# Optimization experiments

Hardware: AMD Instinct MI355X
Metric: run time of the kernel (lower is better)

## Reference

```python
import jax, jax.numpy as jnp
import numpy as np

N = 100000     # total nodes in batch
E = 1600000    # total edges in batch
G = 1024       # number of graphs in batch
IN, H1, H2, FC, OUT = 128, 128, 128, 128, 1


def setup_inputs() -> dict:
    key = jax.random.key(0)
    ks = jax.random.split(key, 8)
    node_feats = jax.random.normal(ks[0], (N, IN), jnp.float32)
    adj = jax.random.randint(ks[1], (2, E), 0, N)
    graph_idx = jnp.sort(jax.random.randint(ks[2], (N,), 0, G))
    init = lambda k, sh, fan: jax.random.normal(k, sh, jnp.float32) / np.float32(np.sqrt(fan))
    W1 = init(ks[3], (IN, H1), IN); b1 = jnp.zeros((H1,), jnp.float32)
    W2 = init(ks[4], (H1, H2), H1); b2 = jnp.zeros((H2,), jnp.float32)
    Wfc = init(ks[5], (H2, FC), H2); bfc = jnp.zeros((FC,), jnp.float32)
    Wout = init(ks[6], (FC, OUT), FC); bout = jnp.zeros((OUT,), jnp.float32)
    return dict(node_feats=node_feats, adj=adj, graph_idx=graph_idx, is_training=0,
                W1=W1, b1=b1, W2=W2, b2=b2, Wfc=Wfc, bfc=bfc, Wout=Wout, bout=bout)


def _gcn_layer(x, src, dst, W, b):
    # h = relu( D^{-1/2} A D^{-1/2} (x W + b) ), A given as an edge list (src -> dst)
    h = x @ W + b                                   # [N, H]
    ones = jnp.ones((src.shape[0],), h.dtype)
    deg = jax.ops.segment_sum(ones, dst, num_segments=N)      # node degrees
    norm = jnp.where(deg > 0, jax.lax.rsqrt(jnp.maximum(deg, 1.0)), 0.0)
    msg = h[src] * norm[src][:, None]               # gather over edges [E, H]
    agg = jax.ops.segment_sum(msg, dst, num_segments=N) * norm[:, None]
    return jax.nn.relu(agg)


def reference(node_feats, adj, graph_idx, is_training, W1, b1, W2, b2, Wfc, bfc, Wout, bout):
    src, dst = adj[0], adj[1]
    h = _gcn_layer(node_feats, src, dst, W1, b1)
    h = _gcn_layer(h, src, dst, W2, b2)
    # mean pooling per graph (segment mean)
    counts = jax.ops.segment_sum(jnp.ones((N,), h.dtype), graph_idx, num_segments=G)
    graph_feat = jax.ops.segment_sum(h, graph_idx, num_segments=G) / jnp.maximum(counts, 1.0)[:, None]
    # MLP head (predicator_dropout = 0.0, is_training=False -> no dropout)
    graph_feat = jax.nn.relu(graph_feat @ Wfc + bfc)
    return graph_feat @ Wout + bout                 # [G, n_out]
```

## Files before the change

### kernel.cpp

```cpp
#include <hip/hip_runtime.h>


typedef unsigned short ushort_t;
typedef unsigned int   uint_t;
typedef unsigned char  uchar_t;
typedef __attribute__((ext_vector_type(8))) short bf16x8;
typedef __attribute__((ext_vector_type(4))) float f32x4;
typedef __attribute__((ext_vector_type(2))) float f32x2;

#define EPB     4096
#define CAP2    32
#define BKT_CAP 8192

__device__ __forceinline__ float bf2f(uint_t u) { return __uint_as_float(u << 16); }
__device__ __forceinline__ ushort_t f2bf(float f) {
  uint_t x = __float_as_uint(f);
  x = x + 0x7fffu + ((x >> 16) & 1u);
  return (ushort_t)(x >> 16);
}

__device__ __forceinline__ bf16x8 pack8(float4 u, float4 v) {
  union { uint4 q; bf16x8 b; } cv;
  cv.q.x = (uint_t)f2bf(u.x) | ((uint_t)f2bf(u.y) << 16);
  cv.q.y = (uint_t)f2bf(u.z) | ((uint_t)f2bf(u.w) << 16);
  cv.q.z = (uint_t)f2bf(v.x) | ((uint_t)f2bf(v.y) << 16);
  cv.q.w = (uint_t)f2bf(v.z) | ((uint_t)f2bf(v.w) << 16);
  return cv.b;
}

__global__ __launch_bounds__(256, 4) void k_front(const float* __restrict__ X, const float* __restrict__ W1,
                                                  const float* __restrict__ b1, uchar_t* __restrict__ Yf8,
                                                  uchar_t* __restrict__ YfC,
                                                  const float* __restrict__ W2, ushort_t* __restrict__ Wf2,
                                                  const int* __restrict__ src, const int* __restrict__ dst,
                                                  uint_t* __restrict__ binbuf, int* __restrict__ cntmatT,
                                                  int E, int N, int nblk, int nbkt, int GB1) {
  __shared__ ushort_t Ws[16384];
  __shared__ int cur[512];
  int t = threadIdx.x;
  int bid = blockIdx.x;

  if (bid < nblk) {
    for (int r = t; r < nbkt; r += 256) cur[r] = 0;
    __syncthreads();
    int base = bid * EPB;
#pragma unroll
    for (int j = 0; j < EPB / 256; j++) {
      int e = base + j * 256 + t;
      if (e < E) {
        int s = src[e], d = dst[e];
        int b = d >> 8;
        int p = atomicAdd(&cur[b], 1);
        if (p < CAP2)
          binbuf[((size_t)b * nblk + bid) * CAP2 + p] = (uint_t)s | ((uint_t)(d & 255) << 17);
      }
    }
    __syncthreads();
    for (int r = t; r < nbkt; r += 256) {
      int c = cur[r];
      cntmatT[(size_t)r * nblk + bid] = (c < CAP2) ? c : CAP2;
    }
    return;
  }
  if (bid < nblk + 64) {
    if (bid == nblk && t < 8)  ((uint4*)Yf8)[(size_t)N * 8 + t] = make_uint4(0u, 0u, 0u, 0u);
    if (bid == nblk && t >= 8 && t < 16)
      ((uint4*)YfC)[(size_t)N * 8 + (t - 8)] = make_uint4(0u, 0u, 0u, 0u);
    int idx = (bid - nblk) * 256 + t;
    int n = idx & 127, k = idx >> 7;
    Wf2[((size_t)(k >> 3) * 128 + n) * 8 + (k & 7)] = f2bf(W2[(size_t)k * 128 + n]);
    return;
  }

  {
    const float4* W4 = (const float4*)W1;
#pragma unroll
    for (int i = 0; i < 16; i++) {
      int idx = i * 256 + t;
      int k = idx >> 5;
      int n0 = (idx & 31) * 4;
      float4 v = W4[idx];
      int qb = k >> 3, j = k & 7;
      Ws[((size_t)qb * 128 + n0 + 0) * 8 + j] = f2bf(v.x);
      Ws[((size_t)qb * 128 + n0 + 1) * 8 + j] = f2bf(v.y);
      Ws[((size_t)qb * 128 + n0 + 2) * 8 + j] = f2bf(v.z);
      Ws[((size_t)qb * 128 + n0 + 3) * 8 + j] = f2bf(v.w);
    }
  }
  int r0 = (bid - nblk - 64) * 128;
  int wave = t >> 6, lane = t & 63;
  int ln = lane & 15, quad = lane >> 4;
  int row0 = r0 + wave * 32 + ln;
  int row1 = row0 + 16;
  int cr0 = min(row0, N - 1);
  int cr1 = min(row1, N - 1);

  bf16x8 a0[4], a1[4];
  {
    const float4* Xp = (const float4*)X;
#pragma unroll
    for (int kc = 0; kc < 4; kc++) {
      int q = kc * 4 + quad;
      float4 u0 = Xp[(size_t)cr0 * 32 + q * 2];
      float4 v0 = Xp[(size_t)cr0 * 32 + q * 2 + 1];
      float4 u1 = Xp[(size_t)cr1 * 32 + q * 2];
      float4 v1 = Xp[(size_t)cr1 * 32 + q * 2 + 1];
      a0[kc] = pack8(u0, v0);
      a1[kc] = pack8(u1, v1);
    }
  }
  __syncthreads();

  const bf16x8* Wb = (const bf16x8*)Ws;
  f32x4 acc[2][8];
#pragma unroll
  for (int mt = 0; mt < 2; mt++)
#pragma unroll
    for (int ct = 0; ct < 8; ct++) acc[mt][ct] = (f32x4){0.f, 0.f, 0.f, 0.f};

#pragma unroll
  for (int kc = 0; kc < 4; kc++) {
    int q = kc * 4 + quad;
#pragma unroll
    for (int ct = 0; ct < 8; ct++) {
      bf16x8 b = Wb[q * 128 + ct * 16 + ln];
      acc[0][ct] = __builtin_amdgcn_mfma_f32_16x16x32_bf16(b, a0[kc], acc[0][ct], 0, 0, 0);
      acc[1][ct] = __builtin_amdgcn_mfma_f32_16x16x32_bf16(b, a1[kc], acc[1][ct], 0, 0, 0);
    }
  }

  int chbase = quad * 4;
  float4 bs[8];
#pragma unroll
  for (int ct = 0; ct < 8; ct++) bs[ct] = *(const float4*)(b1 + ct * 16 + chbase);
  uint_t* Y32 = (uint_t*)Yf8;
  if (row0 < N) {
#pragma unroll
    for (int ct = 0; ct < 8; ct++) {
      f32x4 v = acc[0][ct];
      float x0 = (v[0] + bs[ct].x) * 16.f, x1 = (v[1] + bs[ct].y) * 16.f;
      float x2 = (v[2] + bs[ct].z) * 16.f, x3 = (v[3] + bs[ct].w) * 16.f;
      int w = __builtin_amdgcn_cvt_pk_fp8_f32(x0, x1, 0, false);
      w = __builtin_amdgcn_cvt_pk_fp8_f32(x2, x3, w, true);
      Y32[(size_t)row0 * 32 + ct * 4 + quad] = (uint_t)w;
    }
  }
  if (row1 < N) {
#pragma unroll
    for (int ct = 0; ct < 8; ct++) {
      f32x4 v = acc[1][ct];
      float x0 = (v[0] + bs[ct].x) * 16.f, x1 = (v[1] + bs[ct].y) * 16.f;
      float x2 = (v[2] + bs[ct].z) * 16.f, x3 = (v[3] + bs[ct].w) * 16.f;
      int w = __builtin_amdgcn_cvt_pk_fp8_f32(x0, x1, 0, false);
      w = __builtin_amdgcn_cvt_pk_fp8_f32(x2, x3, w, true);
      Y32[(size_t)row1 * 32 + ct * 4 + quad] = (uint_t)w;
    }
  }
}

__global__ __launch_bounds__(512) void k_csr(const uint_t* __restrict__ binbuf, const int* __restrict__ cntmatT,
                                             int* __restrict__ esrc, int* __restrict__ deg,
                                             int* __restrict__ offs, float* __restrict__ nrm,
                                             int N, int nblk) {
  __shared__ int cnt_s[512];
  __shared__ int hist[256];
  __shared__ int cur[256];
  __shared__ int wsum[4];
  __shared__ int lsrc[BKT_CAP];
  int b = blockIdx.x, t = threadIdx.x;
  if (b == 0 && t == 0) nrm[N] = 0.f;
  int n0 = b << 8;
  int gbase = b * BKT_CAP;
  for (int r = t; r < nblk; r += 512) cnt_s[r] = cntmatT[(size_t)b * nblk + r];
  if (t < 256) hist[t] = 0;
  __syncthreads();
  const uint4* seg4 = (const uint4*)(binbuf + (size_t)b * nblk * CAP2);
  int total4 = (nblk * CAP2) >> 2;
  for (int i4 = t; i4 < total4; i4 += 512) {
    int base = i4 << 2;
    int c = cnt_s[base >> 5];
    int s0 = base & 31;
    if (s0 < c) {
      uint4 v = seg4[i4];
      int nv = c - s0;
      atomicAdd(&hist[v.x >> 17], 1);
      if (nv > 1) atomicAdd(&hist[v.y >> 17], 1);
      if (nv > 2) atomicAdd(&hist[v.z >> 17], 1);
      if (nv > 3) atomicAdd(&hist[v.w >> 17], 1);
    }
  }
  __syncthreads();
  int lane = t & 63, wv = t >> 6;
  if (t < 256) {
    int h = hist[t];
    int incl = h;
#pragma unroll
    for (int s = 1; s < 64; s <<= 1) {
      int x = __shfl_up(incl, s, 64);
      if (lane >= s) incl += x;
    }
    if (lane == 63) wsum[wv] = incl;
    __syncthreads();
    int wbase = 0;
#pragma unroll
    for (int k = 0; k < 4; k++) wbase += (k < wv) ? wsum[k] : 0;
    int excl = wbase + incl - h;
    cur[t] = excl;
    int node = n0 + t;
    if (node < N) {
      deg[node] = h;
      offs[node] = gbase + excl;
      nrm[node] = (h > 0) ? rsqrtf((float)h) : 0.f;
    }
  } else {
    __syncthreads();
  }
  __syncthreads();
  int count = wsum[0] + wsum[1] + wsum[2] + wsum[3];
  for (int i4 = t; i4 < total4; i4 += 512) {
    int base = i4 << 2;
    int c = cnt_s[base >> 5];
    int s0 = base & 31;
    if (s0 < c) {
      uint4 v = seg4[i4];
      int nv = c - s0;
      { int p = atomicAdd(&cur[v.x >> 17], 1); lsrc[p] = (int)(v.x & 0x1ffffu); }
      if (nv > 1) { int p = atomicAdd(&cur[v.y >> 17], 1); lsrc[p] = (int)(v.y & 0x1ffffu); }
      if (nv > 2) { int p = atomicAdd(&cur[v.z >> 17], 1); lsrc[p] = (int)(v.z & 0x1ffffu); }
      if (nv > 3) { int p = atomicAdd(&cur[v.w >> 17], 1); lsrc[p] = (int)(v.w & 0x1ffffu); }
    }
  }
  __syncthreads();
  for (int i = t; i < count; i += 512) esrc[gbase + i] = lsrc[i];
}

__device__ __forceinline__ void acc16p(f32x2* a, uint4 g) {
  a[0] += __builtin_amdgcn_cvt_pk_f32_fp8((int)g.x, false);
  a[1] += __builtin_amdgcn_cvt_pk_f32_fp8((int)g.x, true);
  a[2] += __builtin_amdgcn_cvt_pk_f32_fp8((int)g.y, false);
  a[3] += __builtin_amdgcn_cvt_pk_f32_fp8((int)g.y, true);
  a[4] += __builtin_amdgcn_cvt_pk_f32_fp8((int)g.z, false);
  a[5] += __builtin_amdgcn_cvt_pk_f32_fp8((int)g.z, true);
  a[6] += __builtin_amdgcn_cvt_pk_f32_fp8((int)g.w, false);
  a[7] += __builtin_amdgcn_cvt_pk_f32_fp8((int)g.w, true);
}
__device__ __forceinline__ void acc16f(f32x2* a, uint4 g, float s) {
  f32x2 sv = {s, s};
  a[0] += __builtin_amdgcn_cvt_pk_f32_fp8((int)g.x, false) * sv;
  a[1] += __builtin_amdgcn_cvt_pk_f32_fp8((int)g.x, true)  * sv;
  a[2] += __builtin_amdgcn_cvt_pk_f32_fp8((int)g.y, false) * sv;
  a[3] += __builtin_amdgcn_cvt_pk_f32_fp8((int)g.y, true)  * sv;
  a[4] += __builtin_amdgcn_cvt_pk_f32_fp8((int)g.z, false) * sv;
  a[5] += __builtin_amdgcn_cvt_pk_f32_fp8((int)g.z, true)  * sv;
  a[6] += __builtin_amdgcn_cvt_pk_f32_fp8((int)g.w, false) * sv;
  a[7] += __builtin_amdgcn_cvt_pk_f32_fp8((int)g.w, true)  * sv;
}
__device__ __forceinline__ uint_t pk2(f32x2 v, float nv) {
  float a = fmaxf(v.x * nv, 0.f);
  float b = fmaxf(v.y * nv, 0.f);
  return (uint_t)f2bf(a) | ((uint_t)f2bf(b) << 16);
}

__global__ __launch_bounds__(256, 5) void k_aggemm(const uint4* __restrict__ hn8, const int* __restrict__ offs,
                                                   const int* __restrict__ deg, const float* __restrict__ nrm,
                                                   const int* __restrict__ esrc, const ushort_t* __restrict__ Wf2,
                                                   const float* __restrict__ b2, uchar_t* __restrict__ YfC,
                                                   int N) {
  __shared__ uint4 Hs[32 * 17];
  int wave = threadIdx.x >> 6, lane = threadIdx.x & 63;
  int sub = lane >> 3, sl = lane & 7;
  int base = blockIdx.x * 32;
  int node = base + wave * 8 + sub;
  bool live = node < N;
  int d  = live ? deg[node] : 0;
  int eb = live ? offs[node] : 0;
  int maxd = d;
  maxd = max(maxd, __shfl_xor(maxd, 8, 64));
  maxd = max(maxd, __shfl_xor(maxd, 16, 64));
  maxd = max(maxd, __shfl_xor(maxd, 32, 64));
  f32x2 A[8] = {};
  f32x2 B[8] = {};
  int it = 0;
  for (; it + 4 <= maxd; it += 4) {
    int x0 = esrc[eb + it];
    int x1 = esrc[eb + it + 1];
    int x2 = esrc[eb + it + 2];
    int x3 = esrc[eb + it + 3];
    x0 = (it < d) ? x0 : N;
    x1 = (it + 1 < d) ? x1 : N;
    x2 = (it + 2 < d) ? x2 : N;
    x3 = (it + 3 < d) ? x3 : N;
    uint4 g0 = hn8[(size_t)x0 * 8 + sl];
    uint4 g1 = hn8[(size_t)x1 * 8 + sl];
    uint4 g2 = hn8[(size_t)x2 * 8 + sl];
    uint4 g3 = hn8[(size_t)x3 * 8 + sl];
    float s0 = nrm[x0], s1 = nrm[x1], s2 = nrm[x2], s3 = nrm[x3];
    acc16f(A, g0, s0); acc16f(B, g1, s1);
    acc16f(A, g2, s2); acc16f(B, g3, s3);
  }
  for (; it < maxd; it += 2) {
    int x0 = esrc[eb + it];
    int x1 = esrc[eb + it + 1];
    x0 = (it < d) ? x0 : N;
    x1 = (it + 1 < d) ? x1 : N;
    uint4 g0 = hn8[(size_t)x0 * 8 + sl];
    uint4 g1 = hn8[(size_t)x1 * 8 + sl];
    float s0 = nrm[x0], s1 = nrm[x1];
    acc16f(A, g0, s0); acc16f(B, g1, s1);
  }
  float nv = nrm[live ? node : N] * 0.0625f;
  uint4 p0, p1;
  p0.x = pk2(A[0] + B[0], nv); p0.y = pk2(A[1] + B[1], nv);
  p0.z = pk2(A[2] + B[2], nv); p0.w = pk2(A[3] + B[3], nv);
  p1.x = pk2(A[4] + B[4], nv); p1.y = pk2(A[5] + B[5], nv);
  p1.z = pk2(A[6] + B[6], nv); p1.w = pk2(A[7] + B[7], nv);
  int lrow = wave * 8 + sub;
  Hs[lrow * 17 + sl * 2]     = p0;
  Hs[lrow * 17 + sl * 2 + 1] = p1;
  __syncthreads();

  int ln = lane & 15, quad = lane >> 4;
  const bf16x8* Wb = (const bf16x8*)Wf2;
  f32x4 acc[2][2];
#pragma unroll
  for (int mt = 0; mt < 2; mt++)
#pragma unroll
    for (int c = 0; c < 2; c++) acc[mt][c] = (f32x4){0.f, 0.f, 0.f, 0.f};
#pragma unroll
  for (int kc = 0; kc < 4; kc++) {
    int q = kc * 4 + quad;
    union { uint4 u; bf16x8 b; } a0, a1;
    a0.u = Hs[ln * 17 + q];
    a1.u = Hs[(16 + ln) * 17 + q];
    bf16x8 b0 = Wb[q * 128 + (wave * 2 + 0) * 16 + ln];
    bf16x8 b1 = Wb[q * 128 + (wave * 2 + 1) * 16 + ln];
    acc[0][0] = __builtin_amdgcn_mfma_f32_16x16x32_bf16(b0, a0.b, acc[0][0], 0, 0, 0);
    acc[1][0] = __builtin_amdgcn_mfma_f32_16x16x32_bf16(b0, a1.b, acc[1][0], 0, 0, 0);
    acc[0][1] = __builtin_amdgcn_mfma_f32_16x16x32_bf16(b1, a0.b, acc[0][1], 0, 0, 0);
    acc[1][1] = __builtin_amdgcn_mfma_f32_16x16x32_bf16(b1, a1.b, acc[1][1], 0, 0, 0);
  }
  uint_t* Y32 = (uint_t*)YfC;
#pragma unroll
  for (int mt = 0; mt < 2; mt++) {
    int row = base + mt * 16 + ln;
    int crw = min(row, N);
    float nvr = nrm[crw] * 16.f;
#pragma unroll
    for (int c = 0; c < 2; c++) {
      int ct = wave * 2 + c;
      float4 bs = *(const float4*)(b2 + ct * 16 + quad * 4);
      f32x4 v = acc[mt][c];
      float x0 = (v[0] + bs.x) * nvr, x1 = (v[1] + bs.y) * nvr;
      float x2 = (v[2] + bs.z) * nvr, x3 = (v[3] + bs.w) * nvr;
      int w = __builtin_amdgcn_cvt_pk_fp8_f32(x0, x1, 0, false);
      w = __builtin_amdgcn_cvt_pk_fp8_f32(x2, x3, w, true);
      if (row < N) Y32[(size_t)row * 32 + ct * 4 + quad] = (uint_t)w;
    }
  }
}

__global__ __launch_bounds__(256) void k_agg2(const uint4* __restrict__ hn8, const int* __restrict__ offs,
                                              const int* __restrict__ deg, const float* __restrict__ nrm,
                                              const int* __restrict__ esrc, uint4* __restrict__ outb, int N) {
  int wave = threadIdx.x >> 6, lane = threadIdx.x & 63;
  int sub = lane >> 3, sl = lane & 7;
  int node = blockIdx.x * 32 + wave * 8 + sub;
  bool live = node < N;
  int d  = live ? deg[node] : 0;
  int eb = live ? offs[node] : 0;
  int maxd = d;
  maxd = max(maxd, __shfl_xor(maxd, 8, 64));
  maxd = max(maxd, __shfl_xor(maxd, 16, 64));
  maxd = max(maxd, __shfl_xor(maxd, 32, 64));
  f32x2 A[8] = {};
  f32x2 B[8] = {};
  int it = 0;
  for (; it + 4 <= maxd; it += 4) {
    int x0 = esrc[eb + it];
    int x1 = esrc[eb + it + 1];
    int x2 = esrc[eb + it + 2];
    int x3 = esrc[eb + it + 3];
    x0 = (it < d) ? x0 : N;
    x1 = (it + 1 < d) ? x1 : N;
    x2 = (it + 2 < d) ? x2 : N;
    x3 = (it + 3 < d) ? x3 : N;
    uint4 g0 = hn8[(size_t)x0 * 8 + sl];
    uint4 g1 = hn8[(size_t)x1 * 8 + sl];
    uint4 g2 = hn8[(size_t)x2 * 8 + sl];
    uint4 g3 = hn8[(size_t)x3 * 8 + sl];
    acc16p(A, g0); acc16p(B, g1);
    acc16p(A, g2); acc16p(B, g3);
  }
  for (; it < maxd; it += 2) {
    int x0 = esrc[eb + it];
    int x1 = esrc[eb + it + 1];
    x0 = (it < d) ? x0 : N;
    x1 = (it + 1 < d) ? x1 : N;
    uint4 g0 = hn8[(size_t)x0 * 8 + sl];
    uint4 g1 = hn8[(size_t)x1 * 8 + sl];
    acc16p(A, g0); acc16p(B, g1);
  }
  if (!live) return;
  float nv = nrm[node] * 0.0625f;
  uint4 p0, p1;
  p0.x = pk2(A[0] + B[0], nv); p0.y = pk2(A[1] + B[1], nv);
  p0.z = pk2(A[2] + B[2], nv); p0.w = pk2(A[3] + B[3], nv);
  p1.x = pk2(A[4] + B[4], nv); p1.y = pk2(A[5] + B[5], nv);
  p1.z = pk2(A[6] + B[6], nv); p1.w = pk2(A[7] + B[7], nv);
  outb[(size_t)node * 16 + sl * 2]     = p0;
  outb[(size_t)node * 16 + sl * 2 + 1] = p1;
}

__device__ __forceinline__ int lowerb(const int* __restrict__ a, int n, int v) {
  int lo = 0, hi = n;
  while (lo < hi) { int m = (lo + hi) >> 1; if (a[m] < v) lo = m + 1; else hi = m; }
  return lo;
}

__global__ __launch_bounds__(256) void k_head(const ushort_t* __restrict__ h2, const int* __restrict__ gidx,
                                              const float* __restrict__ Wfc, const float* __restrict__ bfc,
                                              const float* __restrict__ Wout, const float* __restrict__ bout,
                                              float* __restrict__ out, int N) {
  __shared__ float partial[4][128];
  __shared__ float pv[128];
  __shared__ float fcp[2][128];
  __shared__ float red[128];
  __shared__ int segb[2];
  int g = blockIdx.x, t = threadIdx.x;
  int wave = t >> 6, lane = t & 63;
  if (t == 0)  segb[0] = lowerb(gidx, N, g);
  if (t == 64) segb[1] = lowerb(gidx, N, g + 1);
  __syncthreads();
  int lo = segb[0], hi = segb[1];
  int q = lane & 15;
  int r4 = lane >> 4;
  const uint4* h4 = (const uint4*)h2;
  f32x2 A[4] = {};
  for (int i = lo + wave * 4 + r4; i < hi; i += 16) {
    uint4 v = h4[(size_t)i * 16 + q];
    A[0] += (f32x2){__uint_as_float(v.x << 16), __uint_as_float(v.x & 0xffff0000u)};
    A[1] += (f32x2){__uint_as_float(v.y << 16), __uint_as_float(v.y & 0xffff0000u)};
    A[2] += (f32x2){__uint_as_float(v.z << 16), __uint_as_float(v.z & 0xffff0000u)};
    A[3] += (f32x2){__uint_as_float(v.w << 16), __uint_as_float(v.w & 0xffff0000u)};
  }
#pragma unroll
  for (int k = 0; k < 4; k++) {
    A[k].x += __shfl_xor(A[k].x, 16, 64); A[k].y += __shfl_xor(A[k].y, 16, 64);
    A[k].x += __shfl_xor(A[k].x, 32, 64); A[k].y += __shfl_xor(A[k].y, 32, 64);
  }
  if (lane < 16) {
    partial[wave][q * 8 + 0] = A[0].x; partial[wave][q * 8 + 1] = A[0].y;
    partial[wave][q * 8 + 2] = A[1].x; partial[wave][q * 8 + 3] = A[1].y;
    partial[wave][q * 8 + 4] = A[2].x; partial[wave][q * 8 + 5] = A[2].y;
    partial[wave][q * 8 + 6] = A[3].x; partial[wave][q * 8 + 7] = A[3].y;
  }
  __syncthreads();
  if (t < 128) {
    float c = (float)(hi - lo); if (c < 1.f) c = 1.f;
    float s = (partial[0][t] + partial[1][t]) + (partial[2][t] + partial[3][t]);
    pv[t] = s / c;
  }
  __syncthreads();
  int col = t & 127, half = t >> 7;
  float acc = (half == 0) ? bfc[col] : 0.f;
  const float* Wc = Wfc + (size_t)half * 64 * 128 + col;
#pragma unroll 8
  for (int k = 0; k < 64; k++) acc += pv[half * 64 + k] * Wc[k * 128];
  fcp[half][col] = acc;
  __syncthreads();
  if (t < 128) {
    float a = fmaxf(fcp[0][t] + fcp[1][t], 0.f);
    red[t] = a * Wout[t];
  }
  __syncthreads();
  if (t < 64) {
    float v2 = red[t] + red[t + 64];
#pragma unroll
    for (int s = 32; s > 0; s >>= 1) v2 += __shfl_xor(v2, s, 64);
    if (t == 0) out[g] = v2 + bout[0];
  }
}


extern "C" void kernel_launch(void* const* d_in, const int* in_sizes, int n_in,
                              void* d_out, int out_size, void* d_ws, size_t ws_size,
                              hipStream_t stream) {
  const float* X    = (const float*)d_in[0];
  const int*   adj  = (const int*)d_in[1];
  const int*   gidx = (const int*)d_in[2];
  const float* W1   = (const float*)d_in[4];
  const float* b1   = (const float*)d_in[5];
  const float* W2   = (const float*)d_in[6];
  const float* b2   = (const float*)d_in[7];
  const float* Wfc  = (const float*)d_in[8];
  const float* bfc  = (const float*)d_in[9];
  const float* Wout = (const float*)d_in[10];
  const float* bout = (const float*)d_in[11];
  (void)n_in; (void)ws_size;

  const int N = in_sizes[2];
  const int E = in_sizes[1] / 2;
  const int G = out_size;
  const int* srcv = adj;
  const int* dstv = adj + E;
  const int nbkt = (N + 255) >> 8;
  const int nblk = (E + EPB - 1) / EPB;
  const int GB1  = (N + 127) / 128;

  char* w = (char*)d_ws;
  size_t off = 0;
  auto alloc = [&](size_t bytes) -> void* {
    void* p = (void*)(w + off);
    off += (bytes + 255) & ~(size_t)255;
    return p;
  };
  uchar_t*  bufA  = (uchar_t*)alloc((size_t)(N + 1) * 128);
  uchar_t*  bufC  = (uchar_t*)alloc((size_t)(N + 1) * 128);
  ushort_t* bufB  = (ushort_t*)alloc((size_t)N * 128 * sizeof(ushort_t));
  float*    nrm   = (float*)alloc((size_t)(N + 1) * sizeof(float));
  int*      deg   = (int*)alloc((size_t)N * sizeof(int));
  int*      offs  = (int*)alloc((size_t)N * sizeof(int));
  int*      esrc  = (int*)alloc(((size_t)nbkt * BKT_CAP + BKT_CAP) * sizeof(int));
  uint_t*   binb  = (uint_t*)alloc((size_t)nbkt * nblk * CAP2 * sizeof(uint_t));
  int*      cmatT = (int*)alloc((size_t)nbkt * nblk * sizeof(int));
  ushort_t* Wf2   = (ushort_t*)alloc((size_t)128 * 128 * sizeof(ushort_t));

  k_front<<<nblk + 64 + GB1, 256, 0, stream>>>(X, W1, b1, bufA, bufC, W2, Wf2,
                                               srcv, dstv, binb, cmatT,
                                               E, N, nblk, nbkt, GB1);
  k_csr<<<nbkt, 512, 0, stream>>>(binb, cmatT, esrc, deg, offs, nrm, N, nblk);

  const int aggGrid = (N + 31) / 32;
  k_aggemm<<<aggGrid, 256, 0, stream>>>((const uint4*)bufA, offs, deg, nrm, esrc,
                                        Wf2, b2, bufC, N);
  k_agg2<<<aggGrid, 256, 0, stream>>>((const uint4*)bufC, offs, deg, nrm, esrc, (uint4*)bufB, N);
  k_head<<<G, 256, 0, stream>>>(bufB, gidx, Wfc, bfc, Wout, bout, (float*)d_out, N);
}
```

Measured before the change: 246.6 us.

## Move layer-1 GEMM from binning kernel into CSR-build kernel with 512 threads

Splits edge binning into its own kernel and folds the layer-1 transform GEMM and W2 conversion into the CSR-build kernel, which now runs with 512-thread blocks covering 256 rows each. Shared memory is unioned between the CSR scratch and the bf16 W1 tile. The aim is to let the compute-heavy GEMM blocks overlap with the latency-bound CSR blocks instead of with binning. In exchange, the GEMM blocks lose the 4-blocks-per-CU launch bound and each carries the large CSR shared allocation, which may lower occupancy.

```diff
diff --git a/kernel.cpp b/kernel.cpp
--- a/kernel.cpp
+++ b/kernel.cpp
@@ -28,45 +28,126 @@
   return cv.b;
 }
 
-__global__ __launch_bounds__(256, 4) void k_front(const float* __restrict__ X, const float* __restrict__ W1,
-                                                  const float* __restrict__ b1, uchar_t* __restrict__ Yf8,
-                                                  uchar_t* __restrict__ YfC,
-                                                  const float* __restrict__ W2, ushort_t* __restrict__ Wf2,
-                                                  const int* __restrict__ src, const int* __restrict__ dst,
-                                                  uint_t* __restrict__ binbuf, int* __restrict__ cntmatT,
-                                                  int E, int N, int nblk, int nbkt, int GB1) {
-  __shared__ ushort_t Ws[16384];
+__global__ __launch_bounds__(256) void k_bin(const int* __restrict__ src, const int* __restrict__ dst,
+                                             uint_t* __restrict__ binbuf, int* __restrict__ cntmatT,
+                                             int E, int nblk, int nbkt) {
   __shared__ int cur[512];
+  int t = threadIdx.x, bid = blockIdx.x;
+  for (int r = t; r < nbkt; r += 256) cur[r] = 0;
+  __syncthreads();
+  int base = bid * EPB;
+#pragma unroll
+  for (int j = 0; j < EPB / 256; j++) {
+    int e = base + j * 256 + t;
+    if (e < E) {
+      int s = src[e], d = dst[e];
+      int b = d >> 8;
+      int p = atomicAdd(&cur[b], 1);
+      if (p < CAP2)
+        binbuf[((size_t)b * nblk + bid) * CAP2 + p] = (uint_t)s | ((uint_t)(d & 255) << 17);
+    }
+  }
+  __syncthreads();
+  for (int r = t; r < nbkt; r += 256) {
+    int c = cur[r];
+    cntmatT[(size_t)r * nblk + bid] = (c < CAP2) ? c : CAP2;
+  }
+}
+
+__global__ __launch_bounds__(512) void k_mid(const uint_t* __restrict__ binbuf, const int* __restrict__ cntmatT,
+                                             int* __restrict__ esrc, int* __restrict__ deg,
+                                             int* __restrict__ offs, float* __restrict__ nrm,
+                                             const float* __restrict__ X, const float* __restrict__ W1,
+                                             const float* __restrict__ b1, uchar_t* __restrict__ Yf8,
+                                             uchar_t* __restrict__ YfC,
+                                             const float* __restrict__ W2, ushort_t* __restrict__ Wf2,
+                                             int N, int nblk, int nbkt, int GB1m) {
+  __shared__ union {
+    struct {
+      int cnt_s[512];
+      int hist[256];
+      int cur[256];
+      int wsum[4];
+      int lsrc[BKT_CAP];
+    } c;
+    ushort_t Ws[16384];
+  } S;
   int t = threadIdx.x;
   int bid = blockIdx.x;
 
-  if (bid < nblk) {
-    for (int r = t; r < nbkt; r += 256) cur[r] = 0;
+  if (bid < nbkt) {
+    int b = bid;
+    if (b == 0 && t == 0) nrm[N] = 0.f;
+    int n0 = b << 8;
+    int gbase = b * BKT_CAP;
+    for (int r = t; r < nblk; r += 512) S.c.cnt_s[r] = cntmatT[(size_t)b * nblk + r];
+    if (t < 256) S.c.hist[t] = 0;
     __syncthreads();
-    int base = bid * EPB;
-#pragma unroll
-    for (int j = 0; j < EPB / 256; j++) {
-      int e = base + j * 256 + t;
-      if (e < E) {
-        int s = src[e], d = dst[e];
-        int b = d >> 8;
-        int p = atomicAdd(&cur[b], 1);
-        if (p < CAP2)
-          binbuf[((size_t)b * nblk + bid) * CAP2 + p] = (uint_t)s | ((uint_t)(d & 255) << 17);
+    const uint4* seg4 = (const uint4*)(binbuf + (size_t)b * nblk * CAP2);
+    int total4 = (nblk * CAP2) >> 2;
+    for (int i4 = t; i4 < total4; i4 += 512) {
+      int base = i4 << 2;
+      int c = S.c.cnt_s[base >> 5];
+      int s0 = base & 31;
+      if (s0 < c) {
+        uint4 v = seg4[i4];
+        int nv = c - s0;
+        atomicAdd(&S.c.hist[v.x >> 17], 1);
+        if (nv > 1) atomicAdd(&S.c.hist[v.y >> 17], 1);
+        if (nv > 2) atomicAdd(&S.c.hist[v.z >> 17], 1);
+        if (nv > 3) atomicAdd(&S.c.hist[v.w >> 17], 1);
       }
     }
     __syncthreads();
-    for (int r = t; r < nbkt; r += 256) {
-      int c = cur[r];
-      cntmatT[(size_t)r * nblk + bid] = (c < CAP2) ? c : CAP2;
-    }
+    int lane = t & 63, wv = t >> 6;
+    if (t < 256) {
+      int h = S.c.hist[t];
+      int incl = h;
+#pragma unroll
+      for (int s = 1; s < 64; s <<= 1) {
+        int x = __shfl_up(incl, s, 64);
+        if (lane >= s) incl += x;
+      }
+      if (lane == 63) S.c.wsum[wv] = incl;
+      __syncthreads();
+      int wbase = 0;
+#pragma unroll
+      for (int k = 0; k < 4; k++) wbase += (k < wv) ? S.c.wsum[k] : 0;
+      int excl = wbase + incl - h;
+      S.c.cur[t] = excl;
+      int node = n0 + t;
+      if (node < N) {
+        deg[node] = h;
+        offs[node] = gbase + excl;
+        nrm[node] = (h > 0) ? rsqrtf((float)h) : 0.f;
+      }
+    } else {
+      __syncthreads();
+    }
+    __syncthreads();
+    int count = S.c.wsum[0] + S.c.wsum[1] + S.c.wsum[2] + S.c.wsum[3];
+    for (int i4 = t; i4 < total4; i4 += 512) {
+      int base = i4 << 2;
+      int c = S.c.cnt_s[base >> 5];
+      int s0 = base & 31;
+      if (s0 < c) {
+        uint4 v = seg4[i4];
+        int nv = c - s0;
+        { int p = atomicAdd(&S.c.cur[v.x >> 17], 1); S.c.lsrc[p] = (int)(v.x & 0x1ffffu); }
+        if (nv > 1) { int p = atomicAdd(&S.c.cur[v.y >> 17], 1); S.c.lsrc[p] = (int)(v.y & 0x1ffffu); }
+        if (nv > 2) { int p = atomicAdd(&S.c.cur[v.z >> 17], 1); S.c.lsrc[p] = (int)(v.z & 0x1ffffu); }
+        if (nv > 3) { int p = atomicAdd(&S.c.cur[v.w >> 17], 1); S.c.lsrc[p] = (int)(v.w & 0x1ffffu); }
+      }
+    }
+    __syncthreads();
+    for (int i = t; i < count; i += 512) esrc[gbase + i] = S.c.lsrc[i];
     return;
   }
-  if (bid < nblk + 64) {
-    if (bid == nblk && t < 8)  ((uint4*)Yf8)[(size_t)N * 8 + t] = make_uint4(0u, 0u, 0u, 0u);
-    if (bid == nblk && t >= 8 && t < 16)
+  if (bid < nbkt + 32) {
+    if (bid == nbkt && t < 8)  ((uint4*)Yf8)[(size_t)N * 8 + t] = make_uint4(0u, 0u, 0u, 0u);
+    if (bid == nbkt && t >= 8 && t < 16)
       ((uint4*)YfC)[(size_t)N * 8 + (t - 8)] = make_uint4(0u, 0u, 0u, 0u);
-    int idx = (bid - nblk) * 256 + t;
+    int idx = (bid - nbkt) * 512 + t;
     int n = idx & 127, k = idx >> 7;
     Wf2[((size_t)(k >> 3) * 128 + n) * 8 + (k & 7)] = f2bf(W2[(size_t)k * 128 + n]);
     return;
@@ -75,19 +156,19 @@
   {
     const float4* W4 = (const float4*)W1;
 #pragma unroll
-    for (int i = 0; i < 16; i++) {
-      int idx = i * 256 + t;
+    for (int i = 0; i < 8; i++) {
+      int idx = i * 512 + t;
       int k = idx >> 5;
       int n0 = (idx & 31) * 4;
       float4 v = W4[idx];
       int qb = k >> 3, j = k & 7;
-      Ws[((size_t)qb * 128 + n0 + 0) * 8 + j] = f2bf(v.x);
-      Ws[((size_t)qb * 128 + n0 + 1) * 8 + j] = f2bf(v.y);
-      Ws[((size_t)qb * 128 + n0 + 2) * 8 + j] = f2bf(v.z);
-      Ws[((size_t)qb * 128 + n0 + 3) * 8 + j] = f2bf(v.w);
-    }
-  }
-  int r0 = (bid - nblk - 64) * 128;
+      S.Ws[((size_t)qb * 128 + n0 + 0) * 8 + j] = f2bf(v.x);
+      S.Ws[((size_t)qb * 128 + n0 + 1) * 8 + j] = f2bf(v.y);
+      S.Ws[((size_t)qb * 128 + n0 + 2) * 8 + j] = f2bf(v.z);
+      S.Ws[((size_t)qb * 128 + n0 + 3) * 8 + j] = f2bf(v.w);
+    }
+  }
+  int r0 = (bid - nbkt - 32) * 256;
   int wave = t >> 6, lane = t & 63;
   int ln = lane & 15, quad = lane >> 4;
   int row0 = r0 + wave * 32 + ln;
@@ -111,7 +192,7 @@
   }
   __syncthreads();
 
-  const bf16x8* Wb = (const bf16x8*)Ws;
+  const bf16x8* Wb = (const bf16x8*)S.Ws;
   f32x4 acc[2][8];
 #pragma unroll
   for (int mt = 0; mt < 2; mt++)
@@ -156,82 +237,6 @@
       Y32[(size_t)row1 * 32 + ct * 4 + quad] = (uint_t)w;
     }
   }
-}
-
-__global__ __launch_bounds__(512) void k_csr(const uint_t* __restrict__ binbuf, const int* __restrict__ cntmatT,
-                                             int* __restrict__ esrc, int* __restrict__ deg,
-                                             int* __restrict__ offs, float* __restrict__ nrm,
-                                             int N, int nblk) {
-  __shared__ int cnt_s[512];
-  __shared__ int hist[256];
-  __shared__ int cur[256];
-  __shared__ int wsum[4];
-  __shared__ int lsrc[BKT_CAP];
-  int b = blockIdx.x, t = threadIdx.x;
-  if (b == 0 && t == 0) nrm[N] = 0.f;
-  int n0 = b << 8;
-  int gbase = b * BKT_CAP;
-  for (int r = t; r < nblk; r += 512) cnt_s[r] = cntmatT[(size_t)b * nblk + r];
-  if (t < 256) hist[t] = 0;
-  __syncthreads();
-  const uint4* seg4 = (const uint4*)(binbuf + (size_t)b * nblk * CAP2);
-  int total4 = (nblk * CAP2) >> 2;
-  for (int i4 = t; i4 < total4; i4 += 512) {
-    int base = i4 << 2;
-    int c = cnt_s[base >> 5];
-    int s0 = base & 31;
-    if (s0 < c) {
-      uint4 v = seg4[i4];
-      int nv = c - s0;
-      atomicAdd(&hist[v.x >> 17], 1);
-      if (nv > 1) atomicAdd(&hist[v.y >> 17], 1);
-      if (nv > 2) atomicAdd(&hist[v.z >> 17], 1);
-      if (nv > 3) atomicAdd(&hist[v.w >> 17], 1);
-    }
-  }
-  __syncthreads();
-  int lane = t & 63, wv = t >> 6;
-  if (t < 256) {
-    int h = hist[t];
-    int incl = h;
-#pragma unroll
-    for (int s = 1; s < 64; s <<= 1) {
-      int x = __shfl_up(incl, s, 64);
-      if (lane >= s) incl += x;
-    }
-    if (lane == 63) wsum[wv] = incl;
-    __syncthreads();
-    int wbase = 0;
-#pragma unroll
-    for (int k = 0; k < 4; k++) wbase += (k < wv) ? wsum[k] : 0;
-    int excl = wbase + incl - h;
-    cur[t] = excl;
-    int node = n0 + t;
-    if (node < N) {
-      deg[node] = h;
-      offs[node] = gbase + excl;
-      nrm[node] = (h > 0) ? rsqrtf((float)h) : 0.f;
-    }
-  } else {
-    __syncthreads();
-  }
-  __syncthreads();
-  int count = wsum[0] + wsum[1] + wsum[2] + wsum[3];
-  for (int i4 = t; i4 < total4; i4 += 512) {
-    int base = i4 << 2;
-    int c = cnt_s[base >> 5];
-    int s0 = base & 31;
-    if (s0 < c) {
-      uint4 v = seg4[i4];
-      int nv = c - s0;
-      { int p = atomicAdd(&cur[v.x >> 17], 1); lsrc[p] = (int)(v.x & 0x1ffffu); }
-      if (nv > 1) { int p = atomicAdd(&cur[v.y >> 17], 1); lsrc[p] = (int)(v.y & 0x1ffffu); }
-      if (nv > 2) { int p = atomicAdd(&cur[v.z >> 17], 1); lsrc[p] = (int)(v.z & 0x1ffffu); }
-      if (nv > 3) { int p = atomicAdd(&cur[v.w >> 17], 1); lsrc[p] = (int)(v.w & 0x1ffffu); }
-    }
-  }
-  __syncthreads();
-  for (int i = t; i < count; i += 512) esrc[gbase + i] = lsrc[i];
 }
 
 __device__ __forceinline__ void acc16p(f32x2* a, uint4 g) {
@@ -505,7 +510,7 @@
   const int* dstv = adj + E;
   const int nbkt = (N + 255) >> 8;
   const int nblk = (E + EPB - 1) / EPB;
-  const int GB1  = (N + 127) / 128;
+  const int GB1m = (N + 255) / 256;
 
   char* w = (char*)d_ws;
   size_t off = 0;
@@ -525,10 +530,10 @@
   int*      cmatT = (int*)alloc((size_t)nbkt * nblk * sizeof(int));
   ushort_t* Wf2   = (ushort_t*)alloc((size_t)128 * 128 * sizeof(ushort_t));
 
-  k_front<<<nblk + 64 + GB1, 256, 0, stream>>>(X, W1, b1, bufA, bufC, W2, Wf2,
-                                               srcv, dstv, binb, cmatT,
-                                               E, N, nblk, nbkt, GB1);
-  k_csr<<<nbkt, 512, 0, stream>>>(binb, cmatT, esrc, deg, offs, nrm, N, nblk);
+  k_bin<<<nblk, 256, 0, stream>>>(srcv, dstv, binb, cmatT, E, nblk, nbkt);
+  k_mid<<<nbkt + 32 + GB1m, 512, 0, stream>>>(binb, cmatT, esrc, deg, offs, nrm,
+                                              X, W1, b1, bufA, bufC, W2, Wf2,
+                                              N, nblk, nbkt, GB1m);
 
   const int aggGrid = (N + 31) / 32;
   k_aggemm<<<aggGrid, 256, 0, stream>>>((const uint4*)bufA, offs, deg, nrm, esrc,
```

After: 245.2 us (median of 2 runs). Within noise of the previous version (-0.6%).
